# Kernel tuning notes

Hardware: AMD Instinct MI355X
Metric: run time of the kernel (lower is better)

## Reference

```python
import jax, jax.numpy as jnp
import numpy as np

B, T, D, H = 2, 2048, 1024, 16
DH = D // H  # head_dim = 64
ROPE_BASE = 10000.0


def _rope_cos_sin(seq_len, dh, dtype):
    inv_freq = 1.0 / (ROPE_BASE ** (jnp.arange(0, dh, 2, dtype=jnp.float32) / dh))
    t = jnp.arange(seq_len, dtype=jnp.float32)
    freqs = jnp.outer(t, inv_freq)            # [T, dh/2]
    emb = jnp.concatenate([freqs, freqs], -1)  # [T, dh]
    return jnp.cos(emb).astype(dtype), jnp.sin(emb).astype(dtype)


def _rotate_half(x):
    half = x.shape[-1] // 2
    return jnp.concatenate([-x[..., half:], x[..., :half]], axis=-1)


def setup_inputs() -> dict:
    key = jax.random.key(0)
    k1, k2, k3 = jax.random.split(key, 3)
    x = jax.random.normal(k1, (B, T, D), dtype=jnp.float32)
    w_qkv = jax.random.normal(k2, (D, 3 * D), dtype=jnp.float32) * (D ** -0.5)
    w_out = jax.random.normal(k3, (D, D), dtype=jnp.float32) * (D ** -0.5)
    return {"x": x, "w_qkv": w_qkv, "w_out": w_out}


def reference(x, w_qkv, w_out):
    b, t, _ = x.shape
    qkv = x @ w_qkv                                        # [B,T,3D]
    qkv = qkv.reshape(b, t, 3, H, DH).transpose(2, 0, 3, 1, 4)  # [3,B,H,T,DH]
    q, k, v = qkv[0], qkv[1], qkv[2]

    cos, sin = _rope_cos_sin(t, DH, x.dtype)               # [T,DH] each
    q = q * cos + _rotate_half(q) * sin
    k = k * cos + _rotate_half(k) * sin

    scale = DH ** -0.5
    scores = jnp.einsum('bhtd,bhsd->bhts', q, k) * scale   # [B,H,T,T]
    # dense additive causal mask (as in original module)
    neg = jnp.finfo(x.dtype).min
    causal = jnp.triu(jnp.ones((t, t), dtype=bool), k=1)
    scores = scores + jnp.where(causal, neg, jnp.zeros((), x.dtype))
    attn = jax.nn.softmax(scores, axis=-1)
    out = jnp.einsum('bhts,bhsd->bhtd', attn, v)           # [B,H,T,DH]
    out = out.transpose(0, 2, 1, 3).reshape(b, t, D)       # [B,T,D]
    return out @ w_out
```

## Files before the change

kernel.cpp:

```cpp
#include <hip/hip_runtime.h>

typedef __bf16 bf16x8 __attribute__((ext_vector_type(8)));
typedef float f32x4 __attribute__((ext_vector_type(4)));
typedef unsigned int u32x4 __attribute__((ext_vector_type(4)));
typedef unsigned int u32x2 __attribute__((ext_vector_type(2)));
typedef unsigned short u16;
typedef unsigned int u32;

#define BSZ 2
#define TSEQ 2048
#define DMODEL 1024
#define NHEAD 16
#define DHEAD 64

#define GLDS(gp, lp)                                                        \
  __builtin_amdgcn_global_load_lds(                                         \
      (const __attribute__((address_space(1))) void*)(gp),                  \
      (__attribute__((address_space(3))) void*)(lp), 16, 0, 0)

__device__ __forceinline__ u16 f2bf(float f) {
  return __builtin_bit_cast(u16, (__bf16)f);
}
__device__ __forceinline__ float bf2f(u16 h) {
  return __builtin_bit_cast(float, (u32)h << 16);
}

__global__ void k_cvt(const float* __restrict__ in, u16* __restrict__ out, int n4) {
  int i = blockIdx.x * 256 + threadIdx.x;
  if (i >= n4) return;
  float4 v = ((const float4*)in)[i];
  ushort4 o;
  o.x = f2bf(v.x); o.y = f2bf(v.y); o.z = f2bf(v.z); o.w = f2bf(v.w);
  ((ushort4*)out)[i] = o;
}

__global__ void k_transpose_cvt(const float* __restrict__ in, u16* __restrict__ out,
                                int K, int N) {
  __shared__ float tile[64][65];
  int n0 = blockIdx.x * 64, k0 = blockIdx.y * 64;
  int tx = threadIdx.x & 63, ty = threadIdx.x >> 6;
#pragma unroll
  for (int i = ty; i < 64; i += 4)
    tile[i][tx] = in[(size_t)(k0 + i) * N + n0 + tx];
  __syncthreads();
#pragma unroll
  for (int i = ty; i < 64; i += 4)
    out[(size_t)(n0 + i) * K + k0 + tx] = f2bf(tile[tx][i]);
}

__global__ void k_rope_table(float* __restrict__ cosT, float* __restrict__ sinT) {
  int idx = blockIdx.x * 256 + threadIdx.x;
  int t = idx >> 5, f = idx & 31;
  float inv_freq = powf(10000.0f, -(float)(2 * f) / 64.0f);
  float ang = (float)t * inv_freq;
  float s, c;
  sincosf(ang, &s, &c);
  cosT[idx] = c;
  sinT[idx] = s;
}

__device__ __forceinline__ void store_out(u16* C, size_t i, float v) { C[i] = f2bf(v); }
__device__ __forceinline__ void store_out(float* C, size_t i, float v) { C[i] = v; }

template <typename OutT>
__global__ __launch_bounds__(256) void k_gemm(const u16* __restrict__ A,
                                              const u16* __restrict__ Bt,
                                              OutT* __restrict__ C, int M, int N, int K) {
  __shared__ __align__(16) u16 a_lds[2][128][32];
  __shared__ __align__(16) u16 b_lds[2][128][32];
  int m0 = blockIdx.y * 128, n0 = blockIdx.x * 128;
  int tid = threadIdx.x;
  int w = tid >> 6, l = tid & 63, lr = l & 15, lg = l >> 4;
  int wr = (w >> 1) * 64, wc = (w & 1) * 64;
  int grow = l >> 2;
  int gcol = (l & 3) * 8;
  f32x4 acc[4][4] = {};

  const u16* a0 = A + (size_t)(m0 + w * 16 + grow) * K + gcol;
  const u16* a1 = A + (size_t)(m0 + (w + 4) * 16 + grow) * K + gcol;
  const u16* b0 = Bt + (size_t)(n0 + w * 16 + grow) * K + gcol;
  const u16* b1 = Bt + (size_t)(n0 + (w + 4) * 16 + grow) * K + gcol;

  int NT = K >> 5;
  GLDS(a0, &a_lds[0][w * 16][0]);
  GLDS(a1, &a_lds[0][(w + 4) * 16][0]);
  GLDS(b0, &b_lds[0][w * 16][0]);
  GLDS(b1, &b_lds[0][(w + 4) * 16][0]);

  for (int t = 0; t < NT; ++t) {
    int p = t & 1;
    if (t + 1 < NT) {
      int k0 = (t + 1) << 5;
      GLDS(a0 + k0, &a_lds[p ^ 1][w * 16][0]);
      GLDS(a1 + k0, &a_lds[p ^ 1][(w + 4) * 16][0]);
      GLDS(b0 + k0, &b_lds[p ^ 1][w * 16][0]);
      GLDS(b1 + k0, &b_lds[p ^ 1][(w + 4) * 16][0]);
      asm volatile("s_waitcnt vmcnt(4)" ::: "memory");
    } else {
      asm volatile("s_waitcnt vmcnt(0)" ::: "memory");
    }
    __builtin_amdgcn_s_barrier();
    __builtin_amdgcn_sched_barrier(0);
    bf16x8 af[4], bfv[4];
#pragma unroll
    for (int mt = 0; mt < 4; ++mt)
      af[mt] = __builtin_bit_cast(bf16x8, *(const u32x4*)&a_lds[p][wr + mt * 16 + lr][lg * 8]);
#pragma unroll
    for (int nt = 0; nt < 4; ++nt)
      bfv[nt] = __builtin_bit_cast(bf16x8, *(const u32x4*)&b_lds[p][wc + nt * 16 + lr][lg * 8]);
    __builtin_amdgcn_s_setprio(1);
#pragma unroll
    for (int mt = 0; mt < 4; ++mt)
#pragma unroll
      for (int nt = 0; nt < 4; ++nt)
        acc[mt][nt] = __builtin_amdgcn_mfma_f32_16x16x32_bf16(af[mt], bfv[nt], acc[mt][nt], 0, 0, 0);
    __builtin_amdgcn_s_setprio(0);
    __builtin_amdgcn_sched_barrier(0);
    __builtin_amdgcn_s_barrier();
  }

#pragma unroll
  for (int mt = 0; mt < 4; ++mt)
#pragma unroll
    for (int nt = 0; nt < 4; ++nt)
#pragma unroll
      for (int r = 0; r < 4; ++r) {
        int row = m0 + wr + mt * 16 + lg * 4 + r;
        int col = n0 + wc + nt * 16 + lr;
        store_out(C, (size_t)row * N + col, acc[mt][nt][r]);
      }
}

__global__ void k_rope_apply(const u16* __restrict__ qkv, const float* __restrict__ cosT,
                             const float* __restrict__ sinT, u16* __restrict__ Q,
                             u16* __restrict__ K, u16* __restrict__ V) {
  int idx = blockIdx.x * 256 + threadIdx.x;
  int d = idx & 63;
  int t = (idx >> 6) & 2047;
  int h = (idx >> 17) & 15;
  int b = idx >> 21;
  size_t row = (size_t)(b * TSEQ + t) * (3 * DMODEL);
  int cq = h * 64 + d;
  int cp = h * 64 + (d ^ 32);
  float q  = bf2f(qkv[row + cq]);
  float qp = bf2f(qkv[row + cp]);
  float k  = bf2f(qkv[row + DMODEL + cq]);
  float kp = bf2f(qkv[row + DMODEL + cp]);
  float v  = bf2f(qkv[row + 2 * DMODEL + cq]);
  int f = d & 31;
  float c = cosT[t * 32 + f], s = sinT[t * 32 + f];
  float sgn = (d < 32) ? -1.0f : 1.0f;
  float qr = (q * c + sgn * qp * s) * 0.125f;
  float kr = k * c + sgn * kp * s;
  Q[idx] = f2bf(qr);
  K[idx] = f2bf(kr);
  V[idx] = f2bf(v);
}

__global__ __launch_bounds__(256) void k_flash(const u16* __restrict__ Qg, const u16* __restrict__ Kg,
                                               const u16* __restrict__ Vg, u16* __restrict__ O) {
  __shared__ __align__(16) u16 k_lds[64][72];
  __shared__ __align__(16) u16 vsub[4096];
  __shared__ __align__(16) u16 p_lds[4][16][68];
  int pairIdx = blockIdx.x;
  int bh = blockIdx.y;
  int b = bh >> 4, h = bh & 15;
  size_t hoff = (size_t)bh * TSEQ * DHEAD;
  int tid = threadIdx.x, w = tid >> 6, l = tid & 63, lr = l & 15, lg = l >> 4;

  int srow = tid >> 3;
  int g8 = tid & 7;
  int sc8 = g8 * 8;
  u32 vtr = (u32)(uintptr_t)vsub + (u32)(lg * 1024 + lr * 8);

  const u16* kbase = Kg + hoff;
  const u16* vbase = Vg + hoff;

  for (int sub = 0; sub < 2; ++sub) {
    int qb = sub == 0 ? (31 - pairIdx) : pairIdx;

    int qrow = qb * 64 + w * 16 + lr;
    const u16* qp = Qg + hoff + (size_t)qrow * 64 + lg * 8;
    bf16x8 qf0 = __builtin_bit_cast(bf16x8, *(const u32x4*)qp);
    bf16x8 qf1 = __builtin_bit_cast(bf16x8, *(const u32x4*)(qp + 32));

    f32x4 acc[4] = {};
    float mrow[4] = {-1e30f, -1e30f, -1e30f, -1e30f};
    float lrow[4] = {0.f, 0.f, 0.f, 0.f};

    u32x4 kreg[2], vreg[2];
#pragma unroll
    for (int p = 0; p < 2; ++p) {
      int r = srow + p * 32;
      kreg[p] = *(const u32x4*)(kbase + (size_t)r * 64 + sc8);
      vreg[p] = *(const u32x4*)(vbase + (size_t)r * 64 + sc8);
    }

    for (int kv = 0; kv <= qb; ++kv) {
      __syncthreads();
#pragma unroll
      for (int p = 0; p < 2; ++p) {
        int r = srow + p * 32;
        *(u32x4*)&k_lds[r][sc8] = kreg[p];
        int vo = ((r >> 2) * 4 + (g8 >> 1)) * 64 + (r & 3) * 16 + (g8 & 1) * 8;
        *(u32x4*)&vsub[vo] = vreg[p];
      }
      __syncthreads();
      if (kv < qb) {
#pragma unroll
        for (int p = 0; p < 2; ++p) {
          int r = (kv + 1) * 64 + srow + p * 32;
          kreg[p] = *(const u32x4*)(kbase + (size_t)r * 64 + sc8);
          vreg[p] = *(const u32x4*)(vbase + (size_t)r * 64 + sc8);
        }
      }

      f32x4 s[4];
      __builtin_amdgcn_s_setprio(1);
#pragma unroll
      for (int c = 0; c < 4; ++c) {
        const u16* kp2 = &k_lds[c * 16 + lr][lg * 8];
        bf16x8 kf0 = __builtin_bit_cast(bf16x8, *(const u32x4*)kp2);
        bf16x8 kf1 = __builtin_bit_cast(bf16x8, *(const u32x4*)(kp2 + 32));
        f32x4 z = {};
        z = __builtin_amdgcn_mfma_f32_16x16x32_bf16(qf0, kf0, z, 0, 0, 0);
        s[c] = __builtin_amdgcn_mfma_f32_16x16x32_bf16(qf1, kf1, z, 0, 0, 0);
      }
      __builtin_amdgcn_s_setprio(0);
      if (kv == qb) {
#pragma unroll
        for (int c = 0; c < 4; ++c)
#pragma unroll
          for (int r = 0; r < 4; ++r)
            if (c * 16 + lr > w * 16 + lg * 4 + r) s[c][r] = -1e30f;
      }

      float rmax[4], rsum[4];
#pragma unroll
      for (int r = 0; r < 4; ++r)
        rmax[r] = fmaxf(fmaxf(s[0][r], s[1][r]), fmaxf(s[2][r], s[3][r]));
#pragma unroll
      for (int mset = 1; mset <= 8; mset <<= 1)
#pragma unroll
        for (int r = 0; r < 4; ++r)
          rmax[r] = fmaxf(rmax[r], __shfl_xor(rmax[r], mset, 64));
      bool need = (rmax[0] > mrow[0] + 8.0f) | (rmax[1] > mrow[1] + 8.0f) |
                  (rmax[2] > mrow[2] + 8.0f) | (rmax[3] > mrow[3] + 8.0f);
      if (__any(need)) {
        float alpha[4];
#pragma unroll
        for (int r = 0; r < 4; ++r) {
          float mn = fmaxf(mrow[r], rmax[r]);
          alpha[r] = __expf(mrow[r] - mn);
          mrow[r] = mn;
          lrow[r] *= alpha[r];
        }
#pragma unroll
        for (int n = 0; n < 4; ++n)
#pragma unroll
          for (int r = 0; r < 4; ++r)
            acc[n][r] *= alpha[r];
      }
#pragma unroll
      for (int r = 0; r < 4; ++r) rsum[r] = 0.0f;
#pragma unroll
      for (int c = 0; c < 4; ++c)
#pragma unroll
        for (int r = 0; r < 4; ++r) {
          float pe = __expf(s[c][r] - mrow[r]);
          s[c][r] = pe;
          rsum[r] += pe;
        }
#pragma unroll
      for (int mset = 1; mset <= 8; mset <<= 1)
#pragma unroll
        for (int r = 0; r < 4; ++r)
          rsum[r] += __shfl_xor(rsum[r], mset, 64);
#pragma unroll
      for (int r = 0; r < 4; ++r)
        lrow[r] += rsum[r];

#pragma unroll
      for (int c = 0; c < 4; ++c)
#pragma unroll
        for (int r = 0; r < 4; ++r)
          p_lds[w][lg * 4 + r][c * 16 + lr] = f2bf(s[c][r]);
      bf16x8 pa0 = __builtin_bit_cast(bf16x8, *(const u32x4*)&p_lds[w][lr][lg * 8]);
      bf16x8 pa1 = __builtin_bit_cast(bf16x8, *(const u32x4*)&p_lds[w][lr][lg * 8 + 32]);

#pragma unroll
      for (int half = 0; half < 2; ++half) {
        u32x2 t[8];
#pragma unroll
        for (int n2 = 0; n2 < 2; ++n2) {
          int n = half * 2 + n2;
#pragma unroll
          for (int hh = 0; hh < 2; ++hh) {
            u32 alo = vtr + (u32)(hh * 512 + n * 128);
            u32 ahi = alo + 4096;
            asm volatile("ds_read_b64_tr_b16 %0, %1" : "=v"(t[n2 * 4 + hh]) : "v"(alo) : "memory");
            asm volatile("ds_read_b64_tr_b16 %0, %1" : "=v"(t[n2 * 4 + 2 + hh]) : "v"(ahi) : "memory");
          }
        }
        asm volatile("s_waitcnt lgkmcnt(0)" ::: "memory");
        __builtin_amdgcn_sched_barrier(0);
        __builtin_amdgcn_s_setprio(1);
#pragma unroll
        for (int n2 = 0; n2 < 2; ++n2) {
          int n = half * 2 + n2;
          u32x4 vlo, vhi;
          vlo[0] = t[n2 * 4 + 0][0]; vlo[1] = t[n2 * 4 + 0][1];
          vlo[2] = t[n2 * 4 + 1][0]; vlo[3] = t[n2 * 4 + 1][1];
          vhi[0] = t[n2 * 4 + 2][0]; vhi[1] = t[n2 * 4 + 2][1];
          vhi[2] = t[n2 * 4 + 3][0]; vhi[3] = t[n2 * 4 + 3][1];
          acc[n] = __builtin_amdgcn_mfma_f32_16x16x32_bf16(pa0, __builtin_bit_cast(bf16x8, vlo), acc[n], 0, 0, 0);
          acc[n] = __builtin_amdgcn_mfma_f32_16x16x32_bf16(pa1, __builtin_bit_cast(bf16x8, vhi), acc[n], 0, 0, 0);
        }
        __builtin_amdgcn_s_setprio(0);
      }
    }

#pragma unroll
    for (int n = 0; n < 4; ++n)
#pragma unroll
      for (int r = 0; r < 4; ++r) {
        int t = qb * 64 + w * 16 + lg * 4 + r;
        int dd = n * 16 + lr;
        float ov = acc[n][r] / lrow[r];
        O[(size_t)(b * TSEQ + t) * DMODEL + h * 64 + dd] = f2bf(ov);
      }
  }
}

extern "C" void kernel_launch(void* const* d_in, const int* in_sizes, int n_in,
                              void* d_out, int out_size, void* d_ws, size_t ws_size,
                              hipStream_t stream) {
  const float* x     = (const float*)d_in[0];
  const float* w_qkv = (const float*)d_in[1];
  const float* w_out = (const float*)d_in[2];
  float* out = (float*)d_out;

  char* ws = (char*)d_ws;
  size_t off = 0;
  auto alloc = [&](size_t bytes) {
    char* p = ws + off;
    off += (bytes + 255) & ~(size_t)255;
    return p;
  };
  const size_t MT = (size_t)BSZ * TSEQ;
  u16* xb    = (u16*)alloc(MT * DMODEL * 2);
  u16* wqkvT = (u16*)alloc((size_t)3 * DMODEL * DMODEL * 2);
  u16* woutT = (u16*)alloc((size_t)DMODEL * DMODEL * 2);
  u16* qkv   = (u16*)alloc(MT * 3 * DMODEL * 2);
  u16* Qh    = (u16*)alloc(MT * DMODEL * 2);
  u16* Kh    = (u16*)alloc(MT * DMODEL * 2);
  u16* Vh    = (u16*)alloc(MT * DMODEL * 2);
  u16* aout  = (u16*)alloc(MT * DMODEL * 2);
  float* cosT = (float*)alloc((size_t)TSEQ * 32 * 4);
  float* sinT = (float*)alloc((size_t)TSEQ * 32 * 4);
  if (ws_size < off) return;

  k_cvt<<<(MT * DMODEL / 4 + 255) / 256, 256, 0, stream>>>(x, xb, MT * DMODEL / 4);
  k_transpose_cvt<<<dim3(48, 16), 256, 0, stream>>>(w_qkv, wqkvT, DMODEL, 3 * DMODEL);
  k_transpose_cvt<<<dim3(16, 16), 256, 0, stream>>>(w_out, woutT, DMODEL, DMODEL);
  k_rope_table<<<(TSEQ * 32) / 256, 256, 0, stream>>>(cosT, sinT);
  k_gemm<u16><<<dim3(24, 32), 256, 0, stream>>>(xb, wqkvT, qkv, (int)MT, 3 * DMODEL, DMODEL);
  k_rope_apply<<<(int)(MT * DMODEL / 256), 256, 0, stream>>>(qkv, cosT, sinT, Qh, Kh, Vh);
  k_flash<<<dim3(16, BSZ * NHEAD), 256, 0, stream>>>(Qh, Kh, Vh, aout);
  k_gemm<float><<<dim3(8, 32), 256, 0, stream>>>(aout, woutT, out, (int)MT, DMODEL, DMODEL);
}
```

Measured before the change: 231.9 us.

## Fuse RoPE and head scatter into QKV GEMM epilogue; double-buffer flash K/V LDS

```diff
diff --git a/kernel.cpp b/kernel.cpp
--- a/kernel.cpp
+++ b/kernel.cpp
@@ -58,9 +58,6 @@
   cosT[idx] = c;
   sinT[idx] = s;
 }
-
-__device__ __forceinline__ void store_out(u16* C, size_t i, float v) { C[i] = f2bf(v); }
-__device__ __forceinline__ void store_out(float* C, size_t i, float v) { C[i] = v; }
 
 template <typename OutT>
 __global__ __launch_bounds__(256) void k_gemm(const u16* __restrict__ A,
@@ -127,40 +124,102 @@
       for (int r = 0; r < 4; ++r) {
         int row = m0 + wr + mt * 16 + lg * 4 + r;
         int col = n0 + wc + nt * 16 + lr;
-        store_out(C, (size_t)row * N + col, acc[mt][nt][r]);
-      }
-}
-
-__global__ void k_rope_apply(const u16* __restrict__ qkv, const float* __restrict__ cosT,
-                             const float* __restrict__ sinT, u16* __restrict__ Q,
-                             u16* __restrict__ K, u16* __restrict__ V) {
-  int idx = blockIdx.x * 256 + threadIdx.x;
-  int d = idx & 63;
-  int t = (idx >> 6) & 2047;
-  int h = (idx >> 17) & 15;
-  int b = idx >> 21;
-  size_t row = (size_t)(b * TSEQ + t) * (3 * DMODEL);
-  int cq = h * 64 + d;
-  int cp = h * 64 + (d ^ 32);
-  float q  = bf2f(qkv[row + cq]);
-  float qp = bf2f(qkv[row + cp]);
-  float k  = bf2f(qkv[row + DMODEL + cq]);
-  float kp = bf2f(qkv[row + DMODEL + cp]);
-  float v  = bf2f(qkv[row + 2 * DMODEL + cq]);
-  int f = d & 31;
-  float c = cosT[t * 32 + f], s = sinT[t * 32 + f];
-  float sgn = (d < 32) ? -1.0f : 1.0f;
-  float qr = (q * c + sgn * qp * s) * 0.125f;
-  float kr = k * c + sgn * kp * s;
-  Q[idx] = f2bf(qr);
-  K[idx] = f2bf(kr);
-  V[idx] = f2bf(v);
+        C[(size_t)row * N + col] = acc[mt][nt][r];
+      }
+}
+
+__global__ __launch_bounds__(256) void k_gemm_qkv(const u16* __restrict__ A,
+                                                  const u16* __restrict__ Bt,
+                                                  u16* __restrict__ Qh, u16* __restrict__ Kh,
+                                                  u16* __restrict__ Vh,
+                                                  const float* __restrict__ cosT,
+                                                  const float* __restrict__ sinT) {
+  const int M = BSZ * TSEQ, N = 3 * DMODEL, K = DMODEL;
+  __shared__ __align__(16) u16 a_lds[2][128][32];
+  __shared__ __align__(16) u16 b_lds[2][128][32];
+  int m0 = blockIdx.y * 128, n0 = blockIdx.x * 128;
+  int tid = threadIdx.x;
+  int w = tid >> 6, l = tid & 63, lr = l & 15, lg = l >> 4;
+  int wr = (w >> 1) * 64, wc = (w & 1) * 64;
+  int grow = l >> 2;
+  int gcol = (l & 3) * 8;
+  f32x4 acc[4][4] = {};
+
+  const u16* a0 = A + (size_t)(m0 + w * 16 + grow) * K + gcol;
+  const u16* a1 = A + (size_t)(m0 + (w + 4) * 16 + grow) * K + gcol;
+  const u16* b0 = Bt + (size_t)(n0 + w * 16 + grow) * K + gcol;
+  const u16* b1 = Bt + (size_t)(n0 + (w + 4) * 16 + grow) * K + gcol;
+
+  int NT = K >> 5;
+  GLDS(a0, &a_lds[0][w * 16][0]);
+  GLDS(a1, &a_lds[0][(w + 4) * 16][0]);
+  GLDS(b0, &b_lds[0][w * 16][0]);
+  GLDS(b1, &b_lds[0][(w + 4) * 16][0]);
+
+  for (int t = 0; t < NT; ++t) {
+    int p = t & 1;
+    if (t + 1 < NT) {
+      int k0 = (t + 1) << 5;
+      GLDS(a0 + k0, &a_lds[p ^ 1][w * 16][0]);
+      GLDS(a1 + k0, &a_lds[p ^ 1][(w + 4) * 16][0]);
+      GLDS(b0 + k0, &b_lds[p ^ 1][w * 16][0]);
+      GLDS(b1 + k0, &b_lds[p ^ 1][(w + 4) * 16][0]);
+      asm volatile("s_waitcnt vmcnt(4)" ::: "memory");
+    } else {
+      asm volatile("s_waitcnt vmcnt(0)" ::: "memory");
+    }
+    __builtin_amdgcn_s_barrier();
+    __builtin_amdgcn_sched_barrier(0);
+    bf16x8 af[4], bfv[4];
+#pragma unroll
+    for (int mt = 0; mt < 4; ++mt)
+      af[mt] = __builtin_bit_cast(bf16x8, *(const u32x4*)&a_lds[p][wr + mt * 16 + lr][lg * 8]);
+#pragma unroll
+    for (int nt = 0; nt < 4; ++nt)
+      bfv[nt] = __builtin_bit_cast(bf16x8, *(const u32x4*)&b_lds[p][wc + nt * 16 + lr][lg * 8]);
+    __builtin_amdgcn_s_setprio(1);
+#pragma unroll
+    for (int mt = 0; mt < 4; ++mt)
+#pragma unroll
+      for (int nt = 0; nt < 4; ++nt)
+        acc[mt][nt] = __builtin_amdgcn_mfma_f32_16x16x32_bf16(af[mt], bfv[nt], acc[mt][nt], 0, 0, 0);
+    __builtin_amdgcn_s_setprio(0);
+    __builtin_amdgcn_sched_barrier(0);
+    __builtin_amdgcn_s_barrier();
+  }
+
+  int sec = n0 >> 10;
+  int hcol = ((n0 + wc) & 1023) >> 6;
+  u16* outp = (sec == 0) ? Qh : (sec == 1) ? Kh : Vh;
+  float qscale = (sec == 0) ? 0.125f : 1.0f;
+#pragma unroll
+  for (int mt = 0; mt < 4; ++mt)
+#pragma unroll
+    for (int r = 0; r < 4; ++r) {
+      int row = m0 + wr + mt * 16 + lg * 4 + r;
+      int b = row >> 11, tt = row & 2047;
+      size_t obase = ((size_t)((b * 16 + hcol) * 2048 + tt)) * 64;
+      if (sec == 2) {
+#pragma unroll
+        for (int nt = 0; nt < 4; ++nt)
+          outp[obase + nt * 16 + lr] = f2bf(acc[mt][nt][r]);
+      } else {
+        float c0 = cosT[tt * 32 + lr],      s0 = sinT[tt * 32 + lr];
+        float c1 = cosT[tt * 32 + 16 + lr], s1 = sinT[tt * 32 + 16 + lr];
+        float v0 = acc[mt][0][r], v1 = acc[mt][1][r];
+        float v2 = acc[mt][2][r], v3 = acc[mt][3][r];
+        outp[obase + lr]      = f2bf((v0 * c0 - v2 * s0) * qscale);
+        outp[obase + 16 + lr] = f2bf((v1 * c1 - v3 * s1) * qscale);
+        outp[obase + 32 + lr] = f2bf((v2 * c0 + v0 * s0) * qscale);
+        outp[obase + 48 + lr] = f2bf((v3 * c1 + v1 * s1) * qscale);
+      }
+    }
 }
 
 __global__ __launch_bounds__(256) void k_flash(const u16* __restrict__ Qg, const u16* __restrict__ Kg,
                                                const u16* __restrict__ Vg, u16* __restrict__ O) {
-  __shared__ __align__(16) u16 k_lds[64][72];
-  __shared__ __align__(16) u16 vsub[4096];
+  __shared__ __align__(16) u16 k_lds[2][64][72];
+  __shared__ __align__(16) u16 vsub[2][4096];
   __shared__ __align__(16) u16 p_lds[4][16][68];
   int pairIdx = blockIdx.x;
   int bh = blockIdx.y;
@@ -171,7 +230,7 @@
   int srow = tid >> 3;
   int g8 = tid & 7;
   int sc8 = g8 * 8;
-  u32 vtr = (u32)(uintptr_t)vsub + (u32)(lg * 1024 + lr * 8);
+  u32 vtr0 = (u32)(uintptr_t)vsub + (u32)(lg * 1024 + lr * 8);
 
   const u16* kbase = Kg + hoff;
   const u16* vbase = Vg + hoff;
@@ -195,15 +254,16 @@
       kreg[p] = *(const u32x4*)(kbase + (size_t)r * 64 + sc8);
       vreg[p] = *(const u32x4*)(vbase + (size_t)r * 64 + sc8);
     }
+    __syncthreads();
 
     for (int kv = 0; kv <= qb; ++kv) {
-      __syncthreads();
+      int cur = kv & 1;
 #pragma unroll
       for (int p = 0; p < 2; ++p) {
         int r = srow + p * 32;
-        *(u32x4*)&k_lds[r][sc8] = kreg[p];
+        *(u32x4*)&k_lds[cur][r][sc8] = kreg[p];
         int vo = ((r >> 2) * 4 + (g8 >> 1)) * 64 + (r & 3) * 16 + (g8 & 1) * 8;
-        *(u32x4*)&vsub[vo] = vreg[p];
+        *(u32x4*)&vsub[cur][vo] = vreg[p];
       }
       __syncthreads();
       if (kv < qb) {
@@ -219,7 +279,7 @@
       __builtin_amdgcn_s_setprio(1);
 #pragma unroll
       for (int c = 0; c < 4; ++c) {
-        const u16* kp2 = &k_lds[c * 16 + lr][lg * 8];
+        const u16* kp2 = &k_lds[cur][c * 16 + lr][lg * 8];
         bf16x8 kf0 = __builtin_bit_cast(bf16x8, *(const u32x4*)kp2);
         bf16x8 kf1 = __builtin_bit_cast(bf16x8, *(const u32x4*)(kp2 + 32));
         f32x4 z = {};
@@ -288,6 +348,7 @@
       bf16x8 pa0 = __builtin_bit_cast(bf16x8, *(const u32x4*)&p_lds[w][lr][lg * 8]);
       bf16x8 pa1 = __builtin_bit_cast(bf16x8, *(const u32x4*)&p_lds[w][lr][lg * 8 + 32]);
 
+      u32 vtr = vtr0 + (u32)(cur * 8192);
 #pragma unroll
       for (int half = 0; half < 2; ++half) {
         u32x2 t[8];
@@ -351,7 +412,6 @@
   u16* xb    = (u16*)alloc(MT * DMODEL * 2);
   u16* wqkvT = (u16*)alloc((size_t)3 * DMODEL * DMODEL * 2);
   u16* woutT = (u16*)alloc((size_t)DMODEL * DMODEL * 2);
-  u16* qkv   = (u16*)alloc(MT * 3 * DMODEL * 2);
   u16* Qh    = (u16*)alloc(MT * DMODEL * 2);
   u16* Kh    = (u16*)alloc(MT * DMODEL * 2);
   u16* Vh    = (u16*)alloc(MT * DMODEL * 2);
@@ -364,8 +424,7 @@
   k_transpose_cvt<<<dim3(48, 16), 256, 0, stream>>>(w_qkv, wqkvT, DMODEL, 3 * DMODEL);
   k_transpose_cvt<<<dim3(16, 16), 256, 0, stream>>>(w_out, woutT, DMODEL, DMODEL);
   k_rope_table<<<(TSEQ * 32) / 256, 256, 0, stream>>>(cosT, sinT);
-  k_gemm<u16><<<dim3(24, 32), 256, 0, stream>>>(xb, wqkvT, qkv, (int)MT, 3 * DMODEL, DMODEL);
-  k_rope_apply<<<(int)(MT * DMODEL / 256), 256, 0, stream>>>(qkv, cosT, sinT, Qh, Kh, Vh);
+  k_gemm_qkv<<<dim3(24, 32), 256, 0, stream>>>(xb, wqkvT, Qh, Kh, Vh, cosT, sinT);
   k_flash<<<dim3(16, BSZ * NHEAD), 256, 0, stream>>>(Qh, Kh, Vh, aout);
   k_gemm<float><<<dim3(8, 32), 256, 0, stream>>>(aout, woutT, out, (int)MT, DMODEL, DMODEL);
 }
```

New measurement: 225.4 us. 1.03x faster.
